# Kernel optimization log

Hardware: AMD Instinct MI355X
Metric: run time of the kernel (lower is better)

Reference implementation:

```python
import itertools
import jax, jax.numpy as jnp
import numpy as np

NUM_HEADS = 8
KEY_DIM = 32
EXPANDED_KEY_DIM = 128  # attention_ratio(4) * key_dim(32)
RESOLUTION = 7
DIM = 448
HIDDEN = (KEY_DIM * 2 + EXPANDED_KEY_DIM) * NUM_HEADS  # 1536


def _build_bias_idxs(resolution: int) -> np.ndarray:
    points = list(itertools.product(range(resolution), range(resolution)))
    attention_offsets = {}
    idxs = []
    for p1 in points:
        for p2 in points:
            offset = (abs(p1[0] - p2[0]), abs(p1[1] - p2[1]))
            if offset not in attention_offsets:
                attention_offsets[offset] = len(attention_offsets)
            idxs.append(attention_offsets[offset])
    n = len(points)
    return np.array(idxs, dtype=np.int64).reshape(n, n)


def setup_inputs() -> dict:
    key = jax.random.key(0)
    ks = jax.random.split(key, 6)
    B, S = 2048, RESOLUTION * RESOLUTION
    return {
        "hidden_states": jax.random.normal(ks[0], (B, S, DIM), dtype=jnp.float32),
        "qkv_w": jax.random.normal(ks[1], (HIDDEN, DIM), dtype=jnp.float32) * 0.02,
        "qkv_b": jax.random.normal(ks[2], (HIDDEN,), dtype=jnp.float32) * 0.02,
        "proj_w": jax.random.normal(ks[3], (DIM, EXPANDED_KEY_DIM * NUM_HEADS), dtype=jnp.float32) * 0.02,
        "proj_b": jax.random.normal(ks[4], (DIM,), dtype=jnp.float32) * 0.02,
        "attention_biases": jax.random.normal(ks[5], (NUM_HEADS, 49), dtype=jnp.float32) * 0.02,
        "bias_idxs": jnp.asarray(_build_bias_idxs(RESOLUTION)),
    }


def reference(hidden_states, qkv_w, qkv_b, proj_w, proj_b, attention_biases, bias_idxs):
    B, S, C = hidden_states.shape
    scale = KEY_DIM ** -0.5
    # fused QKV projection then split per head
    qkv = hidden_states @ qkv_w.T + qkv_b                      # [B,S,1536]
    qkv = qkv.reshape(B, S, NUM_HEADS, KEY_DIM * 2 + EXPANDED_KEY_DIM)
    q = qkv[..., :KEY_DIM]                                     # [B,S,H,32]
    k = qkv[..., KEY_DIM:2 * KEY_DIM]                          # [B,S,H,32]
    v = qkv[..., 2 * KEY_DIM:]                                 # [B,S,H,128]
    bias = attention_biases[:, bias_idxs]                      # [H,S,S] gathered rel-pos bias
    scores = jnp.einsum('bqhd,bkhd->bhqk', q, k) * scale + bias
    probs = jax.nn.softmax(scores, axis=-1)                    # [B,H,S,S]
    ctx = jnp.einsum('bhqk,bkhd->bqhd', probs, v)              # [B,S,H,128]
    ctx = ctx.reshape(B, S, NUM_HEADS * EXPANDED_KEY_DIM)
    return ctx @ proj_w.T + proj_b                             # [B,S,448]
```

## Files before the change

### kernel.cpp

```cpp
#include <hip/hip_runtime.h>
#include <hip/hip_bf16.h>
#include <cstdint>

using bf16 = __hip_bfloat16;
using bf16x8 = __attribute__((ext_vector_type(8))) short;
using f32x4  = __attribute__((ext_vector_type(4))) float;

#define NHEADS 8
#define SEQ 49
#define CDIM 448
#define PDIM 1024
#define QS 36
#define VTS 68
#define CS 132

static constexpr int SM_CTX = 0;
static constexpr int SM_QL  = 16896;
static constexpr int SM_KL  = 21504;
static constexpr int SM_VT  = 26112;
static constexpr int SM_AB  = 43520;
static constexpr int SM_SZ  = 45088;

static constexpr size_t kNhs = (size_t)2048 * SEQ * CDIM;
static constexpr size_t kNqw = (size_t)1536 * CDIM;
static constexpr size_t kNqb = 1536;
static constexpr size_t kNpw = (size_t)CDIM * PDIM;
static constexpr size_t kNpb = CDIM;
static constexpr size_t kNab = NHEADS * SEQ;
static constexpr size_t OFF_HS = 64;
static constexpr size_t OFF_QW = OFF_HS + kNhs * 2;
static constexpr size_t OFF_QB = OFF_QW + kNqw * 2;
static constexpr size_t OFF_PW = OFF_QB + kNqb * 2;
static constexpr size_t OFF_PB = OFF_PW + kNpw * 2;
static constexpr size_t OFF_AB = OFF_PB + kNpb * 2;
static constexpr size_t WS_NEEDED = OFF_AB + kNab * 2;

__device__ __forceinline__ short f2s(float x) {
    union { bf16 h; short s; } u; u.h = __float2bfloat16(x); return u.s;
}
__device__ __forceinline__ bf16x8 load8(const bf16* p) { return *(const bf16x8*)p; }
__device__ __forceinline__ bf16x8 load8(const float* p) {
    f32x4 a = *(const f32x4*)p;
    f32x4 b = *(const f32x4*)(p + 4);
    bf16x8 r;
    r[0]=f2s(a[0]); r[1]=f2s(a[1]); r[2]=f2s(a[2]); r[3]=f2s(a[3]);
    r[4]=f2s(b[0]); r[5]=f2s(b[1]); r[6]=f2s(b[2]); r[7]=f2s(b[3]);
    return r;
}
__device__ __forceinline__ float toF(bf16 x) { return __bfloat162float(x); }
__device__ __forceinline__ float toF(float x) { return x; }
__device__ __forceinline__ void storeT(bf16* p, float v) { *p = __float2bfloat16(v); }
__device__ __forceinline__ void storeT(float* p, float v) { *p = v; }

__device__ __forceinline__ void cvt_arr(const float* __restrict__ src,
                                        bf16* __restrict__ dst, size_t n4,
                                        size_t tid, size_t np) {
    for (size_t i = tid; i < n4; i += np) {
        f32x4 v = ((const f32x4*)src)[i];
        short4 o;
        o.x = f2s(v[0]); o.y = f2s(v[1]); o.z = f2s(v[2]); o.w = f2s(v[3]);
        ((short4*)dst)[i] = o;
    }
}

__global__ void convert_inputs(const float* hs, const float* qw, const float* qb,
                               const float* pw, const float* pb, const float* ab,
                               unsigned char* ws, const int* flag) {
    if (*flag == 0) return;
    const size_t tid = (size_t)blockIdx.x * blockDim.x + threadIdx.x;
    const size_t np  = (size_t)gridDim.x * blockDim.x;
    cvt_arr(hs, (bf16*)(ws + OFF_HS), kNhs / 4, tid, np);
    cvt_arr(qw, (bf16*)(ws + OFF_QW), kNqw / 4, tid, np);
    cvt_arr(qb, (bf16*)(ws + OFF_QB), kNqb / 4, tid, np);
    cvt_arr(pw, (bf16*)(ws + OFF_PW), kNpw / 4, tid, np);
    cvt_arr(pb, (bf16*)(ws + OFF_PB), kNpb / 4, tid, np);
    cvt_arr(ab, (bf16*)(ws + OFF_AB), kNab / 4, tid, np);
}

template <typename T, typename TO>
__device__ __forceinline__
void body(const T* __restrict__ hs, const T* __restrict__ qkv_w,
          const T* __restrict__ qkv_b, const T* __restrict__ proj_w,
          const T* __restrict__ proj_b, const T* __restrict__ ab,
          TO* __restrict__ out, char* smem) {
    bf16*  ctxp = (bf16*)(smem + SM_CTX);
    bf16*  ql   = (bf16*)(smem + SM_QL);
    bf16*  kl   = (bf16*)(smem + SM_KL);
    bf16*  vtl  = (bf16*)(smem + SM_VT);
    float* abl  = (float*)(smem + SM_AB);

    const int b   = blockIdx.x;
    const int tid = threadIdx.x;
    const int l   = tid & 63;
    const int w   = tid >> 6;
    const int lr  = l & 15;
    const int lk  = (l >> 4) * 8;
    const int cm  = (l >> 4) * 4;
    const int cn  = l & 15;

    for (int i = tid; i < NHEADS * SEQ; i += 256) abl[i] = toF(ab[i]);
    for (int i = tid; i < 128 * (64 - SEQ); i += 256) {
        const int d = i / (64 - SEQ), t = SEQ + i % (64 - SEQ);
        vtl[d * VTS + t] = __float2bfloat16(0.f);
    }

    int rq[4], rr[4], cq[4], cr[4];
    #pragma unroll
    for (int r = 0; r < 4; ++r) {
        int row = 16 * w + cm + r; if (row > SEQ - 1) row = SEQ - 1;
        rq[r] = (row * 37) >> 8; rr[r] = row - rq[r] * 7;
    }
    #pragma unroll
    for (int j = 0; j < 4; ++j) {
        int col = 16 * j + cn; if (col > SEQ - 1) col = 0;
        cq[j] = (col * 37) >> 8; cr[j] = col - cq[j] * 7;
    }

    f32x4 oacc[4][7] = {};
    const float scale = 0.17677669529663687f;
    const T* hsb = hs + (size_t)b * SEQ * CDIM;

    for (int h = 0; h < NHEADS; ++h) {
        f32x4 qacc[3][4] = {};
        bf16x8 af0[4], bf0[3], af1[4], bf1[3];

        auto LOADA = [&](int ks, bf16x8* af, bf16x8* bfr) {
            const int k0 = ks * 32;
            #pragma unroll
            for (int mf = 0; mf < 4; ++mf) {
                int row = 16 * mf + lr; if (row > SEQ - 1) row = SEQ - 1;
                af[mf] = load8(hsb + row * CDIM + k0 + lk);
            }
            #pragma unroll
            for (int j = 0; j < 3; ++j) {
                const int n = h * 192 + (3 * w + j) * 16 + lr;
                bfr[j] = load8(qkv_w + (size_t)n * CDIM + k0 + lk);
            }
        };
        auto MFMAA = [&](bf16x8* af, bf16x8* bfr) {
            #pragma unroll
            for (int j = 0; j < 3; ++j)
                #pragma unroll
                for (int mf = 0; mf < 4; ++mf)
                    qacc[j][mf] = __builtin_amdgcn_mfma_f32_16x16x32_bf16(
                        af[mf], bfr[j], qacc[j][mf], 0, 0, 0);
        };

        LOADA(0, af0, bf0);
        LOADA(1, af1, bf1);
        #pragma unroll
        for (int ks = 0; ks < 14; ks += 2) {
            MFMAA(af0, bf0);
            if (ks + 2 < 14) LOADA(ks + 2, af0, bf0);
            MFMAA(af1, bf1);
            if (ks + 3 < 14) LOADA(ks + 3, af1, bf1);
        }

        #pragma unroll
        for (int j = 0; j < 3; ++j) {
            const int c = (3 * w + j) * 16 + cn;
            const float bv = toF(qkv_b[h * 192 + c]);
            #pragma unroll
            for (int mf = 0; mf < 4; ++mf)
                #pragma unroll
                for (int r = 0; r < 4; ++r) {
                    const int row = 16 * mf + cm + r;
                    const float v = qacc[j][mf][r] + bv;
                    if (row < SEQ) {
                        if (c < 32)      ql[row * QS + c] = __float2bfloat16(v);
                        else if (c < 64) kl[row * QS + (c - 32)] = __float2bfloat16(v);
                        else             vtl[(c - 64) * VTS + row] = __float2bfloat16(v);
                    }
                }
        }
        __syncthreads();

        {
            const bf16x8 aq = *(const bf16x8*)(ql + (16 * w + lr) * QS + lk);
            f32x4 sacc[4] = {};
            #pragma unroll
            for (int j = 0; j < 4; ++j) {
                const bf16x8 kb = *(const bf16x8*)(kl + (16 * j + lr) * QS + lk);
                sacc[j] = __builtin_amdgcn_mfma_f32_16x16x32_bf16(
                    aq, kb, sacc[j], 0, 0, 0);
            }
            #pragma unroll
            for (int r = 0; r < 4; ++r) {
                const int row = 16 * w + cm + r;
                float v[4], e[4];
                float m = -3.0e38f;
                #pragma unroll
                for (int j = 0; j < 4; ++j) {
                    const int col = 16 * j + cn;
                    if (col < SEQ) {
                        int dy = rq[r] - cq[j]; dy = dy < 0 ? -dy : dy;
                        int dx = rr[r] - cr[j]; dx = dx < 0 ? -dx : dx;
                        v[j] = sacc[j][r] * scale + abl[h * SEQ + dy * 7 + dx];
                        m = fmaxf(m, v[j]);
                    } else v[j] = -3.0e38f;
                }
                m = fmaxf(m, __shfl_xor(m, 1));
                m = fmaxf(m, __shfl_xor(m, 2));
                m = fmaxf(m, __shfl_xor(m, 4));
                m = fmaxf(m, __shfl_xor(m, 8));
                float s = 0.f;
                #pragma unroll
                for (int j = 0; j < 4; ++j) {
                    e[j] = (16 * j + cn < SEQ) ? __expf(v[j] - m) : 0.f;
                    s += e[j];
                }
                s += __shfl_xor(s, 1);
                s += __shfl_xor(s, 2);
                s += __shfl_xor(s, 4);
                s += __shfl_xor(s, 8);
                const float inv = 1.f / s;
                #pragma unroll
                for (int j = 0; j < 4; ++j)
                    ctxp[row * CS + 16 * j + cn] = __float2bfloat16(e[j] * inv);
            }
        }

        {
            const bf16x8 pa0 = *(const bf16x8*)(ctxp + (16 * w + lr) * CS + lk);
            const bf16x8 pa1 = *(const bf16x8*)(ctxp + (16 * w + lr) * CS + 32 + lk);
            f32x4 cacc[8] = {};
            #pragma unroll
            for (int n = 0; n < 8; ++n) {
                const bf16x8 vb0 = *(const bf16x8*)(vtl + (16 * n + lr) * VTS + lk);
                cacc[n] = __builtin_amdgcn_mfma_f32_16x16x32_bf16(
                    pa0, vb0, cacc[n], 0, 0, 0);
            }
            #pragma unroll
            for (int n = 0; n < 8; ++n) {
                const bf16x8 vb1 = *(const bf16x8*)(vtl + (16 * n + lr) * VTS + 32 + lk);
                cacc[n] = __builtin_amdgcn_mfma_f32_16x16x32_bf16(
                    pa1, vb1, cacc[n], 0, 0, 0);
            }
            #pragma unroll
            for (int n = 0; n < 8; ++n)
                #pragma unroll
                for (int r = 0; r < 4; ++r)
                    ctxp[(16 * w + cm + r) * CS + 16 * n + cn] =
                        __float2bfloat16(cacc[n][r]);
        }
        __syncthreads();

        #pragma unroll
        for (int ks3 = 0; ks3 < 4; ++ks3) {
            bf16x8 bw[7], ac[4];
            #pragma unroll
            for (int j = 0; j < 7; ++j) {
                const int n = (w * 7 + j) * 16 + lr;
                bw[j] = load8(proj_w + (size_t)n * PDIM + h * 128 + ks3 * 32 + lk);
            }
            #pragma unroll
            for (int mf = 0; mf < 4; ++mf)
                ac[mf] = *(const bf16x8*)(ctxp + (16 * mf + lr) * CS + ks3 * 32 + lk);
            #pragma unroll
            for (int mf = 0; mf < 4; ++mf)
                #pragma unroll
                for (int j = 0; j < 7; ++j)
                    oacc[mf][j] = __builtin_amdgcn_mfma_f32_16x16x32_bf16(
                        ac[mf], bw[j], oacc[mf][j], 0, 0, 0);
        }
    }

    #pragma unroll
    for (int j = 0; j < 7; ++j) {
        const int col = w * 112 + j * 16 + cn;
        const float pbv = toF(proj_b[col]);
        #pragma unroll
        for (int mf = 0; mf < 4; ++mf)
            #pragma unroll
            for (int r = 0; r < 4; ++r) {
                const int row = 16 * mf + cm + r;
                if (row < SEQ)
                    storeT(out + ((size_t)b * SEQ + row) * CDIM + col,
                           oacc[mf][j][r] + pbv);
            }
    }
}

__global__ void detect_dtype(const unsigned int* __restrict__ w, int* __restrict__ flag) {
    if (threadIdx.x == 0 && blockIdx.x == 0) {
        int cnt = 0;
        for (int i = 0; i < 256; ++i) {
            const unsigned e = (w[i] >> 7) & 0xFF;
            cnt += (e >= 0x40 && e <= 0x7D);
        }
        *flag = (cnt < 156) ? 1 : 0;
    }
}

__global__ __launch_bounds__(256, 2)
void fused_effattn(const void* hs, const void* qkv_w, const void* qkv_b,
                   const void* proj_w, const void* proj_b, const void* ab,
                   const int* idxs, void* out, unsigned char* ws, int use_ws) {
    __shared__ __align__(16) char smem[SM_SZ];

    const int f = *(const int*)ws;
    if (f) {
        if (use_ws) {
            body<bf16, float>((const bf16*)(ws + OFF_HS), (const bf16*)(ws + OFF_QW),
                              (const bf16*)(ws + OFF_QB), (const bf16*)(ws + OFF_PW),
                              (const bf16*)(ws + OFF_PB), (const bf16*)(ws + OFF_AB),
                              (float*)out, smem);
        } else {
            body<float, float>((const float*)hs, (const float*)qkv_w,
                               (const float*)qkv_b, (const float*)proj_w,
                               (const float*)proj_b, (const float*)ab,
                               (float*)out, smem);
        }
    } else {
        body<bf16, bf16>((const bf16*)hs, (const bf16*)qkv_w, (const bf16*)qkv_b,
                         (const bf16*)proj_w, (const bf16*)proj_b, (const bf16*)ab,
                         (bf16*)out, smem);
    }
}

extern "C" void kernel_launch(void* const* d_in, const int* in_sizes, int n_in,
                              void* d_out, int out_size, void* d_ws, size_t ws_size,
                              hipStream_t stream) {
    unsigned char* ws = (unsigned char*)d_ws;
    detect_dtype<<<1, 64, 0, stream>>>((const unsigned int*)d_in[1], (int*)ws);
    const int use_ws = (ws_size >= WS_NEEDED) ? 1 : 0;
    if (use_ws)
        convert_inputs<<<dim3(2048), dim3(256), 0, stream>>>(
            (const float*)d_in[0], (const float*)d_in[1], (const float*)d_in[2],
            (const float*)d_in[3], (const float*)d_in[4], (const float*)d_in[5],
            ws, (const int*)ws);
    fused_effattn<<<dim3(2048), dim3(256), 0, stream>>>(
        d_in[0], d_in[1], d_in[2], d_in[3], d_in[4], d_in[5],
        (const int*)d_in[6], d_out, ws, use_ws);
}
```

Before: 1.519 ms.

## Split QKV projection into standalone tiled GEMM, feed attention+proj kernel from workspace

Pulls the QKV projection out of the per-batch fused kernel into a separate 128x128-tiled MFMA GEMM over all 100352 rows. Its bf16 output goes to a workspace buffer, which removes the per-block recomputation pattern and the poor reuse of 49-row tiles. The attention+projection kernel then stages each head's Q/K/V from the workspace, prefetching the next head while the output projection runs. The cost is an extra global round trip for the QKV intermediate, and the split path only runs when the workspace is large enough; otherwise the old fused path is used.

```diff
diff --git a/kernel.cpp b/kernel.cpp
--- a/kernel.cpp
+++ b/kernel.cpp
@@ -10,10 +10,28 @@
 #define SEQ 49
 #define CDIM 448
 #define PDIM 1024
+
+#define MROWS 100352
+#define MTILES 784
+#define NTILES 12
+#define AQKS 72
+#define AVTS 72
+#define ACS 136
+#define OLS 136
+
+static constexpr int SM2_CTX = 0;
+static constexpr int SM2_QK  = 17408;
+static constexpr int SM2_VT  = 24480;
+static constexpr int SM2_AB  = 42912;
+static constexpr int SM2_SZ  = 44480;
+
+static constexpr size_t OFF_QKV   = 64;
+static constexpr size_t QKV_BYTES = (size_t)MROWS * 1536 * 2;
+static constexpr size_t WS_SPLIT  = OFF_QKV + QKV_BYTES;
+
 #define QS 36
 #define VTS 68
 #define CS 132
-
 static constexpr int SM_CTX = 0;
 static constexpr int SM_QL  = 16896;
 static constexpr int SM_KL  = 21504;
@@ -52,42 +70,98 @@
 __device__ __forceinline__ void storeT(bf16* p, float v) { *p = __float2bfloat16(v); }
 __device__ __forceinline__ void storeT(float* p, float v) { *p = v; }
 
-__device__ __forceinline__ void cvt_arr(const float* __restrict__ src,
-                                        bf16* __restrict__ dst, size_t n4,
-                                        size_t tid, size_t np) {
-    for (size_t i = tid; i < n4; i += np) {
-        f32x4 v = ((const f32x4*)src)[i];
-        short4 o;
-        o.x = f2s(v[0]); o.y = f2s(v[1]); o.z = f2s(v[2]); o.w = f2s(v[3]);
-        ((short4*)dst)[i] = o;
-    }
-}
-
-__global__ void convert_inputs(const float* hs, const float* qw, const float* qb,
-                               const float* pw, const float* pb, const float* ab,
-                               unsigned char* ws, const int* flag) {
-    if (*flag == 0) return;
-    const size_t tid = (size_t)blockIdx.x * blockDim.x + threadIdx.x;
-    const size_t np  = (size_t)gridDim.x * blockDim.x;
-    cvt_arr(hs, (bf16*)(ws + OFF_HS), kNhs / 4, tid, np);
-    cvt_arr(qw, (bf16*)(ws + OFF_QW), kNqw / 4, tid, np);
-    cvt_arr(qb, (bf16*)(ws + OFF_QB), kNqb / 4, tid, np);
-    cvt_arr(pw, (bf16*)(ws + OFF_PW), kNpw / 4, tid, np);
-    cvt_arr(pb, (bf16*)(ws + OFF_PB), kNpb / 4, tid, np);
-    cvt_arr(ab, (bf16*)(ws + OFF_AB), kNab / 4, tid, np);
+template <typename T>
+__device__ __forceinline__
+void qkv_gemm_body(const T* __restrict__ hs, const T* __restrict__ qw,
+                   const T* __restrict__ qb, bf16* __restrict__ qkv, bf16* ol) {
+    const int bid = blockIdx.x;
+    const int bn  = bid / MTILES;
+    const int bm  = bid - bn * MTILES;
+    const int tid = threadIdx.x;
+    const int l   = tid & 63;
+    const int w   = tid >> 6;
+    const int wm  = w >> 1, wn = w & 1;
+    const int lr  = l & 15;
+    const int lk  = (l >> 4) * 8;
+    const int cm  = (l >> 4) * 4;
+    const int cn  = l & 15;
+
+    const size_t r0 = (size_t)bm * 128 + wm * 64;
+    const int    c0 = bn * 128 + wn * 64;
+
+    f32x4 acc[4][4] = {};
+    bf16x8 afA[4], bfA[4], afB[4], bfB[4];
+
+    auto LOADG = [&](int ks, bf16x8* af, bf16x8* bfr) {
+        const int k0 = ks * 32;
+        #pragma unroll
+        for (int mf = 0; mf < 4; ++mf)
+            af[mf] = load8(hs + (r0 + 16 * mf + lr) * CDIM + k0 + lk);
+        #pragma unroll
+        for (int nf = 0; nf < 4; ++nf)
+            bfr[nf] = load8(qw + (size_t)(c0 + 16 * nf + lr) * CDIM + k0 + lk);
+    };
+    auto MM = [&](bf16x8* af, bf16x8* bfr) {
+        #pragma unroll
+        for (int mf = 0; mf < 4; ++mf)
+            #pragma unroll
+            for (int nf = 0; nf < 4; ++nf)
+                acc[mf][nf] = __builtin_amdgcn_mfma_f32_16x16x32_bf16(
+                    af[mf], bfr[nf], acc[mf][nf], 0, 0, 0);
+    };
+
+    LOADG(0, afA, bfA);
+    LOADG(1, afB, bfB);
+    #pragma unroll
+    for (int ks = 0; ks < 14; ks += 2) {
+        MM(afA, bfA);
+        if (ks + 2 < 14) LOADG(ks + 2, afA, bfA);
+        MM(afB, bfB);
+        if (ks + 3 < 14) LOADG(ks + 3, afB, bfB);
+    }
+
+    float bv[4];
+    #pragma unroll
+    for (int nf = 0; nf < 4; ++nf)
+        bv[nf] = toF(qb[c0 + 16 * nf + cn]);
+    #pragma unroll
+    for (int mf = 0; mf < 4; ++mf)
+        #pragma unroll
+        for (int nf = 0; nf < 4; ++nf)
+            #pragma unroll
+            for (int r = 0; r < 4; ++r)
+                ol[(wm * 64 + 16 * mf + cm + r) * OLS + wn * 64 + 16 * nf + cn] =
+                    __float2bfloat16(acc[mf][nf][r] + bv[nf]);
+    __syncthreads();
+    for (int p = tid; p < 2048; p += 256) {
+        const int row = p >> 4, c16 = p & 15;
+        *(int4*)(qkv + ((size_t)bm * 128 + row) * 1536 + bn * 128 + c16 * 8) =
+            *(const int4*)(ol + row * OLS + c16 * 8);
+    }
+}
+
+__global__ __launch_bounds__(256, 2)
+void qkv_gemm_k(const void* hs, const void* qw, const void* qb,
+                unsigned char* ws) {
+    __shared__ __align__(16) bf16 ol[128 * OLS];
+    bf16* qkv = (bf16*)(ws + OFF_QKV);
+    if (*(const int*)ws)
+        qkv_gemm_body<float>((const float*)hs, (const float*)qw,
+                             (const float*)qb, qkv, ol);
+    else
+        qkv_gemm_body<bf16>((const bf16*)hs, (const bf16*)qw,
+                            (const bf16*)qb, qkv, ol);
 }
 
 template <typename T, typename TO>
 __device__ __forceinline__
-void body(const T* __restrict__ hs, const T* __restrict__ qkv_w,
-          const T* __restrict__ qkv_b, const T* __restrict__ proj_w,
-          const T* __restrict__ proj_b, const T* __restrict__ ab,
-          TO* __restrict__ out, char* smem) {
-    bf16*  ctxp = (bf16*)(smem + SM_CTX);
-    bf16*  ql   = (bf16*)(smem + SM_QL);
-    bf16*  kl   = (bf16*)(smem + SM_KL);
-    bf16*  vtl  = (bf16*)(smem + SM_VT);
-    float* abl  = (float*)(smem + SM_AB);
+void attn_body(const bf16* __restrict__ qkv, const T* __restrict__ proj_w,
+               const T* __restrict__ proj_b, const T* __restrict__ ab,
+               TO* __restrict__ out, char* smem) {
+    bf16*  ctxp = (bf16*)(smem + SM2_CTX);
+    bf16*  qkl  = (bf16*)(smem + SM2_QK);
+    bf16*  vtl  = (bf16*)(smem + SM2_VT);
+    float* abl  = (float*)(smem + SM2_AB);
 
     const int b   = blockIdx.x;
     const int tid = threadIdx.x;
@@ -101,7 +175,7 @@
     for (int i = tid; i < NHEADS * SEQ; i += 256) abl[i] = toF(ab[i]);
     for (int i = tid; i < 128 * (64 - SEQ); i += 256) {
         const int d = i / (64 - SEQ), t = SEQ + i % (64 - SEQ);
-        vtl[d * VTS + t] = __float2bfloat16(0.f);
+        vtl[d * AVTS + t] = __float2bfloat16(0.f);
     }
 
     int rq[4], rr[4], cq[4], cr[4];
@@ -116,71 +190,55 @@
         cq[j] = (col * 37) >> 8; cr[j] = col - cq[j] * 7;
     }
 
+    const bf16* qb = qkv + (size_t)b * SEQ * 1536;
+
+    int4 qs0, qs1, vs0, vs1, vs2, vs3;
+    auto STAGE_LOAD = [&](int hh) {
+        const bf16* hb = qb + hh * 192;
+        { const int p = tid;       const int t = p >> 3, c = p & 7;
+          qs0 = *(const int4*)(hb + (size_t)t * 1536 + c * 8); }
+        { const int p = tid + 256; if (p < 392) { const int t = p >> 3, c = p & 7;
+          qs1 = *(const int4*)(hb + (size_t)t * 1536 + c * 8); } }
+        { const int p = tid;       const int t = p >> 4, c = p & 15;
+          vs0 = *(const int4*)(hb + (size_t)t * 1536 + 64 + c * 8); }
+        { const int p = tid + 256; const int t = p >> 4, c = p & 15;
+          vs1 = *(const int4*)(hb + (size_t)t * 1536 + 64 + c * 8); }
+        { const int p = tid + 512; const int t = p >> 4, c = p & 15;
+          vs2 = *(const int4*)(hb + (size_t)t * 1536 + 64 + c * 8); }
+        { const int p = tid + 768; if (p < 784) { const int t = p >> 4, c = p & 15;
+          vs3 = *(const int4*)(hb + (size_t)t * 1536 + 64 + c * 8); } }
+    };
+    auto WRV = [&](int p, int4 v) {
+        const int t = p >> 4, c = p & 15;
+        bf16 tmp[8]; *(int4*)tmp = v;
+        #pragma unroll
+        for (int j = 0; j < 8; ++j) vtl[(c * 8 + j) * AVTS + t] = tmp[j];
+    };
+    auto STAGE_WRITE = [&]() {
+        { const int p = tid;       const int t = p >> 3, c = p & 7;
+          *(int4*)(qkl + t * AQKS + c * 8) = qs0; }
+        { const int p = tid + 256; if (p < 392) { const int t = p >> 3, c = p & 7;
+          *(int4*)(qkl + t * AQKS + c * 8) = qs1; } }
+        WRV(tid, vs0); WRV(tid + 256, vs1); WRV(tid + 512, vs2);
+        if (tid < 16) WRV(tid + 768, vs3);
+    };
+
     f32x4 oacc[4][7] = {};
     const float scale = 0.17677669529663687f;
-    const T* hsb = hs + (size_t)b * SEQ * CDIM;
+
+    STAGE_LOAD(0);
+    STAGE_WRITE();
+    __syncthreads();
 
     for (int h = 0; h < NHEADS; ++h) {
-        f32x4 qacc[3][4] = {};
-        bf16x8 af0[4], bf0[3], af1[4], bf1[3];
-
-        auto LOADA = [&](int ks, bf16x8* af, bf16x8* bfr) {
-            const int k0 = ks * 32;
-            #pragma unroll
-            for (int mf = 0; mf < 4; ++mf) {
-                int row = 16 * mf + lr; if (row > SEQ - 1) row = SEQ - 1;
-                af[mf] = load8(hsb + row * CDIM + k0 + lk);
-            }
-            #pragma unroll
-            for (int j = 0; j < 3; ++j) {
-                const int n = h * 192 + (3 * w + j) * 16 + lr;
-                bfr[j] = load8(qkv_w + (size_t)n * CDIM + k0 + lk);
-            }
-        };
-        auto MFMAA = [&](bf16x8* af, bf16x8* bfr) {
-            #pragma unroll
-            for (int j = 0; j < 3; ++j)
-                #pragma unroll
-                for (int mf = 0; mf < 4; ++mf)
-                    qacc[j][mf] = __builtin_amdgcn_mfma_f32_16x16x32_bf16(
-                        af[mf], bfr[j], qacc[j][mf], 0, 0, 0);
-        };
-
-        LOADA(0, af0, bf0);
-        LOADA(1, af1, bf1);
-        #pragma unroll
-        for (int ks = 0; ks < 14; ks += 2) {
-            MFMAA(af0, bf0);
-            if (ks + 2 < 14) LOADA(ks + 2, af0, bf0);
-            MFMAA(af1, bf1);
-            if (ks + 3 < 14) LOADA(ks + 3, af1, bf1);
-        }
-
-        #pragma unroll
-        for (int j = 0; j < 3; ++j) {
-            const int c = (3 * w + j) * 16 + cn;
-            const float bv = toF(qkv_b[h * 192 + c]);
-            #pragma unroll
-            for (int mf = 0; mf < 4; ++mf)
-                #pragma unroll
-                for (int r = 0; r < 4; ++r) {
-                    const int row = 16 * mf + cm + r;
-                    const float v = qacc[j][mf][r] + bv;
-                    if (row < SEQ) {
-                        if (c < 32)      ql[row * QS + c] = __float2bfloat16(v);
-                        else if (c < 64) kl[row * QS + (c - 32)] = __float2bfloat16(v);
-                        else             vtl[(c - 64) * VTS + row] = __float2bfloat16(v);
-                    }
-                }
-        }
-        __syncthreads();
-
         {
-            const bf16x8 aq = *(const bf16x8*)(ql + (16 * w + lr) * QS + lk);
+            const int qrow = (16 * w + lr < SEQ) ? 16 * w + lr : SEQ - 1;
+            const bf16x8 aq = *(const bf16x8*)(qkl + qrow * AQKS + lk);
             f32x4 sacc[4] = {};
             #pragma unroll
             for (int j = 0; j < 4; ++j) {
-                const bf16x8 kb = *(const bf16x8*)(kl + (16 * j + lr) * QS + lk);
+                const int krow = (16 * j + lr < SEQ) ? 16 * j + lr : SEQ - 1;
+                const bf16x8 kb = *(const bf16x8*)(qkl + krow * AQKS + 32 + lk);
                 sacc[j] = __builtin_amdgcn_mfma_f32_16x16x32_bf16(
                     aq, kb, sacc[j], 0, 0, 0);
             }
@@ -216,6 +274,250 @@
                 const float inv = 1.f / s;
                 #pragma unroll
                 for (int j = 0; j < 4; ++j)
+                    ctxp[row * ACS + 16 * j + cn] = __float2bfloat16(e[j] * inv);
+            }
+        }
+
+        {
+            const bf16x8 pa0 = *(const bf16x8*)(ctxp + (16 * w + lr) * ACS + lk);
+            const bf16x8 pa1 = *(const bf16x8*)(ctxp + (16 * w + lr) * ACS + 32 + lk);
+            f32x4 cacc[8] = {};
+            #pragma unroll
+            for (int n = 0; n < 8; ++n) {
+                const bf16x8 vb = *(const bf16x8*)(vtl + (16 * n + lr) * AVTS + lk);
+                cacc[n] = __builtin_amdgcn_mfma_f32_16x16x32_bf16(
+                    pa0, vb, cacc[n], 0, 0, 0);
+            }
+            #pragma unroll
+            for (int n = 0; n < 8; ++n) {
+                const bf16x8 vb = *(const bf16x8*)(vtl + (16 * n + lr) * AVTS + 32 + lk);
+                cacc[n] = __builtin_amdgcn_mfma_f32_16x16x32_bf16(
+                    pa1, vb, cacc[n], 0, 0, 0);
+            }
+            #pragma unroll
+            for (int n = 0; n < 8; ++n)
+                #pragma unroll
+                for (int r = 0; r < 4; ++r)
+                    ctxp[(16 * w + cm + r) * ACS + 16 * n + cn] =
+                        __float2bfloat16(cacc[n][r]);
+        }
+        __syncthreads();
+
+        if (h + 1 < NHEADS) STAGE_LOAD(h + 1);
+        #pragma unroll
+        for (int ks3 = 0; ks3 < 4; ++ks3) {
+            bf16x8 bw[7], ac[4];
+            #pragma unroll
+            for (int j = 0; j < 7; ++j) {
+                const int n = (w * 7 + j) * 16 + lr;
+                bw[j] = load8(proj_w + (size_t)n * PDIM + h * 128 + ks3 * 32 + lk);
+            }
+            #pragma unroll
+            for (int mf = 0; mf < 4; ++mf)
+                ac[mf] = *(const bf16x8*)(ctxp + (16 * mf + lr) * ACS + ks3 * 32 + lk);
+            #pragma unroll
+            for (int mf = 0; mf < 4; ++mf)
+                #pragma unroll
+                for (int j = 0; j < 7; ++j)
+                    oacc[mf][j] = __builtin_amdgcn_mfma_f32_16x16x32_bf16(
+                        ac[mf], bw[j], oacc[mf][j], 0, 0, 0);
+        }
+        if (h + 1 < NHEADS) {
+            STAGE_WRITE();
+            __syncthreads();
+        }
+    }
+
+    #pragma unroll
+    for (int j = 0; j < 7; ++j) {
+        const int col = w * 112 + j * 16 + cn;
+        const float pbv = toF(proj_b[col]);
+        #pragma unroll
+        for (int mf = 0; mf < 4; ++mf)
+            #pragma unroll
+            for (int r = 0; r < 4; ++r) {
+                const int row = 16 * mf + cm + r;
+                if (row < SEQ)
+                    storeT(out + ((size_t)b * SEQ + row) * CDIM + col,
+                           oacc[mf][j][r] + pbv);
+            }
+    }
+}
+
+__global__ __launch_bounds__(256, 2)
+void attn_proj_k(const void* proj_w, const void* proj_b, const void* ab,
+                 void* out, unsigned char* ws) {
+    __shared__ __align__(16) char smem[SM2_SZ];
+    const bf16* qkv = (const bf16*)(ws + OFF_QKV);
+    if (*(const int*)ws)
+        attn_body<float, float>(qkv, (const float*)proj_w, (const float*)proj_b,
+                                (const float*)ab, (float*)out, smem);
+    else
+        attn_body<bf16, bf16>(qkv, (const bf16*)proj_w, (const bf16*)proj_b,
+                              (const bf16*)ab, (bf16*)out, smem);
+}
+
+__device__ __forceinline__ void cvt_arr(const float* __restrict__ src,
+                                        bf16* __restrict__ dst, size_t n4,
+                                        size_t tid, size_t np) {
+    for (size_t i = tid; i < n4; i += np) {
+        f32x4 v = ((const f32x4*)src)[i];
+        short4 o;
+        o.x = f2s(v[0]); o.y = f2s(v[1]); o.z = f2s(v[2]); o.w = f2s(v[3]);
+        ((short4*)dst)[i] = o;
+    }
+}
+
+__global__ void convert_inputs(const float* hs, const float* qw, const float* qb,
+                               const float* pw, const float* pb, const float* ab,
+                               unsigned char* ws, const int* flag) {
+    if (*flag == 0) return;
+    const size_t tid = (size_t)blockIdx.x * blockDim.x + threadIdx.x;
+    const size_t np  = (size_t)gridDim.x * blockDim.x;
+    cvt_arr(hs, (bf16*)(ws + OFF_HS), kNhs / 4, tid, np);
+    cvt_arr(qw, (bf16*)(ws + OFF_QW), kNqw / 4, tid, np);
+    cvt_arr(qb, (bf16*)(ws + OFF_QB), kNqb / 4, tid, np);
+    cvt_arr(pw, (bf16*)(ws + OFF_PW), kNpw / 4, tid, np);
+    cvt_arr(pb, (bf16*)(ws + OFF_PB), kNpb / 4, tid, np);
+    cvt_arr(ab, (bf16*)(ws + OFF_AB), kNab / 4, tid, np);
+}
+
+template <typename T, typename TO>
+__device__ __forceinline__
+void body(const T* __restrict__ hs, const T* __restrict__ qkv_w,
+          const T* __restrict__ qkv_b, const T* __restrict__ proj_w,
+          const T* __restrict__ proj_b, const T* __restrict__ ab,
+          TO* __restrict__ out, char* smem) {
+    bf16*  ctxp = (bf16*)(smem + SM_CTX);
+    bf16*  ql   = (bf16*)(smem + SM_QL);
+    bf16*  kl   = (bf16*)(smem + SM_KL);
+    bf16*  vtl  = (bf16*)(smem + SM_VT);
+    float* abl  = (float*)(smem + SM_AB);
+
+    const int b   = blockIdx.x;
+    const int tid = threadIdx.x;
+    const int l   = tid & 63;
+    const int w   = tid >> 6;
+    const int lr  = l & 15;
+    const int lk  = (l >> 4) * 8;
+    const int cm  = (l >> 4) * 4;
+    const int cn  = l & 15;
+
+    for (int i = tid; i < NHEADS * SEQ; i += 256) abl[i] = toF(ab[i]);
+    for (int i = tid; i < 128 * (64 - SEQ); i += 256) {
+        const int d = i / (64 - SEQ), t = SEQ + i % (64 - SEQ);
+        vtl[d * VTS + t] = __float2bfloat16(0.f);
+    }
+
+    int rq[4], rr[4], cq[4], cr[4];
+    #pragma unroll
+    for (int r = 0; r < 4; ++r) {
+        int row = 16 * w + cm + r; if (row > SEQ - 1) row = SEQ - 1;
+        rq[r] = (row * 37) >> 8; rr[r] = row - rq[r] * 7;
+    }
+    #pragma unroll
+    for (int j = 0; j < 4; ++j) {
+        int col = 16 * j + cn; if (col > SEQ - 1) col = 0;
+        cq[j] = (col * 37) >> 8; cr[j] = col - cq[j] * 7;
+    }
+
+    f32x4 oacc[4][7] = {};
+    const float scale = 0.17677669529663687f;
+    const T* hsb = hs + (size_t)b * SEQ * CDIM;
+
+    for (int h = 0; h < NHEADS; ++h) {
+        f32x4 qacc[3][4] = {};
+        bf16x8 af0[4], bf0[3], af1[4], bf1[3];
+        auto LOADA = [&](int ks, bf16x8* af, bf16x8* bfr) {
+            const int k0 = ks * 32;
+            #pragma unroll
+            for (int mf = 0; mf < 4; ++mf) {
+                int row = 16 * mf + lr; if (row > SEQ - 1) row = SEQ - 1;
+                af[mf] = load8(hsb + row * CDIM + k0 + lk);
+            }
+            #pragma unroll
+            for (int j = 0; j < 3; ++j) {
+                const int n = h * 192 + (3 * w + j) * 16 + lr;
+                bfr[j] = load8(qkv_w + (size_t)n * CDIM + k0 + lk);
+            }
+        };
+        auto MFMAA = [&](bf16x8* af, bf16x8* bfr) {
+            #pragma unroll
+            for (int j = 0; j < 3; ++j)
+                #pragma unroll
+                for (int mf = 0; mf < 4; ++mf)
+                    qacc[j][mf] = __builtin_amdgcn_mfma_f32_16x16x32_bf16(
+                        af[mf], bfr[j], qacc[j][mf], 0, 0, 0);
+        };
+        LOADA(0, af0, bf0);
+        LOADA(1, af1, bf1);
+        #pragma unroll
+        for (int ks = 0; ks < 14; ks += 2) {
+            MFMAA(af0, bf0);
+            if (ks + 2 < 14) LOADA(ks + 2, af0, bf0);
+            MFMAA(af1, bf1);
+            if (ks + 3 < 14) LOADA(ks + 3, af1, bf1);
+        }
+        #pragma unroll
+        for (int j = 0; j < 3; ++j) {
+            const int c = (3 * w + j) * 16 + cn;
+            const float bv = toF(qkv_b[h * 192 + c]);
+            #pragma unroll
+            for (int mf = 0; mf < 4; ++mf)
+                #pragma unroll
+                for (int r = 0; r < 4; ++r) {
+                    const int row = 16 * mf + cm + r;
+                    const float v = qacc[j][mf][r] + bv;
+                    if (row < SEQ) {
+                        if (c < 32)      ql[row * QS + c] = __float2bfloat16(v);
+                        else if (c < 64) kl[row * QS + (c - 32)] = __float2bfloat16(v);
+                        else             vtl[(c - 64) * VTS + row] = __float2bfloat16(v);
+                    }
+                }
+        }
+        __syncthreads();
+
+        {
+            const bf16x8 aq = *(const bf16x8*)(ql + (16 * w + lr) * QS + lk);
+            f32x4 sacc[4] = {};
+            #pragma unroll
+            for (int j = 0; j < 4; ++j) {
+                const bf16x8 kb = *(const bf16x8*)(kl + (16 * j + lr) * QS + lk);
+                sacc[j] = __builtin_amdgcn_mfma_f32_16x16x32_bf16(
+                    aq, kb, sacc[j], 0, 0, 0);
+            }
+            #pragma unroll
+            for (int r = 0; r < 4; ++r) {
+                const int row = 16 * w + cm + r;
+                float v[4], e[4];
+                float m = -3.0e38f;
+                #pragma unroll
+                for (int j = 0; j < 4; ++j) {
+                    const int col = 16 * j + cn;
+                    if (col < SEQ) {
+                        int dy = rq[r] - cq[j]; dy = dy < 0 ? -dy : dy;
+                        int dx = rr[r] - cr[j]; dx = dx < 0 ? -dx : dx;
+                        v[j] = sacc[j][r] * scale + abl[h * SEQ + dy * 7 + dx];
+                        m = fmaxf(m, v[j]);
+                    } else v[j] = -3.0e38f;
+                }
+                m = fmaxf(m, __shfl_xor(m, 1));
+                m = fmaxf(m, __shfl_xor(m, 2));
+                m = fmaxf(m, __shfl_xor(m, 4));
+                m = fmaxf(m, __shfl_xor(m, 8));
+                float s = 0.f;
+                #pragma unroll
+                for (int j = 0; j < 4; ++j) {
+                    e[j] = (16 * j + cn < SEQ) ? __expf(v[j] - m) : 0.f;
+                    s += e[j];
+                }
+                s += __shfl_xor(s, 1);
+                s += __shfl_xor(s, 2);
+                s += __shfl_xor(s, 4);
+                s += __shfl_xor(s, 8);
+                const float inv = 1.f / s;
+                #pragma unroll
+                for (int j = 0; j < 4; ++j)
                     ctxp[row * CS + 16 * j + cn] = __float2bfloat16(e[j] * inv);
             }
         }
@@ -297,7 +599,6 @@
                    const void* proj_w, const void* proj_b, const void* ab,
                    const int* idxs, void* out, unsigned char* ws, int use_ws) {
     __shared__ __align__(16) char smem[SM_SZ];
-
     const int f = *(const int*)ws;
     if (f) {
         if (use_ws) {
@@ -323,13 +624,20 @@
                               hipStream_t stream) {
     unsigned char* ws = (unsigned char*)d_ws;
     detect_dtype<<<1, 64, 0, stream>>>((const unsigned int*)d_in[1], (int*)ws);
-    const int use_ws = (ws_size >= WS_NEEDED) ? 1 : 0;
-    if (use_ws)
-        convert_inputs<<<dim3(2048), dim3(256), 0, stream>>>(
-            (const float*)d_in[0], (const float*)d_in[1], (const float*)d_in[2],
-            (const float*)d_in[3], (const float*)d_in[4], (const float*)d_in[5],
-            ws, (const int*)ws);
-    fused_effattn<<<dim3(2048), dim3(256), 0, stream>>>(
-        d_in[0], d_in[1], d_in[2], d_in[3], d_in[4], d_in[5],
-        (const int*)d_in[6], d_out, ws, use_ws);
-}
+    if (ws_size >= WS_SPLIT) {
+        qkv_gemm_k<<<dim3(MTILES * NTILES), dim3(256), 0, stream>>>(
+            d_in[0], d_in[1], d_in[2], ws);
+        attn_proj_k<<<dim3(2048), dim3(256), 0, stream>>>(
+            d_in[3], d_in[4], d_in[5], d_out, ws);
+    } else {
+        const int use_ws = (ws_size >= WS_NEEDED) ? 1 : 0;
+        if (use_ws)
+            convert_inputs<<<dim3(2048), dim3(256), 0, stream>>>(
+                (const float*)d_in[0], (const float*)d_in[1], (const float*)d_in[2],
+                (const float*)d_in[3], (const float*)d_in[4], (const float*)d_in[5],
+                ws, (const int*)ws);
+        fused_effattn<<<dim3(2048), dim3(256), 0, stream>>>(
+            d_in[0], d_in[1], d_in[2], d_in[3], d_in[4], d_in[5],
+            (const int*)d_in[6], d_out, ws, use_ws);
+    }
+}
```

Result: slower. 2.102 ms (+38.4%).
